# Kernel optimization log

Hardware: AMD Instinct MI355X
Metric: run time of the kernel (lower is better)

## Reference

```python
import jax, jax.numpy as jnp
import numpy as np

MARGIN = 0.2
NEG_SENTINEL = -1e30


def setup_inputs() -> dict:
    key = jax.random.key(0)
    k1, k2 = jax.random.split(key)
    batch_reprs = jax.random.normal(k1, (4096, 128), dtype=jnp.float32)
    batch_labels = jax.random.randint(k2, (4096,), 0, 512, dtype=jnp.int64 if jax.config.jax_enable_x64 else jnp.int32)
    return {"batch_reprs": batch_reprs, "batch_labels": batch_labels}


def _loss(batch_reprs, batch_labels):
    # class match matrix (self-similarity kept, as in original)
    match = (batch_labels[:, None] == batch_labels[None, :]).astype(batch_reprs.dtype)  # [B,B]

    # pairwise euclidean distance (squared=False), sim = -dist
    sq = jnp.sum(batch_reprs * batch_reprs, axis=1)
    d2 = jnp.maximum(sq[:, None] + sq[None, :] - 2.0 * (batch_reprs @ batch_reprs.T), 0.0)
    zero = (d2 == 0.0).astype(batch_reprs.dtype)
    dist = jnp.sqrt(d2 + zero * 1e-16) * (1.0 - zero)
    sim_hat = -dist + (1.0 - match) * MARGIN  # use_margin=True

    # rank positions via double argsort (descending)
    order = jnp.argsort(-sim_hat, axis=1)
    rank = jnp.argsort(order, axis=1).astype(sim_hat.dtype) + 1.0  # [B,B], 1-based ranks

    k = jnp.sum(match, axis=1, keepdims=True)                      # n_pos per row, [B,1]
    fp = (match < 1.0) & (rank <= k)                               # false positives
    fp_num = jnp.sum(fp, axis=1, keepdims=True).astype(sim_hat.dtype)
    fn = (match > 0.0) & (rank > k)                                # false negatives

    n = sim_hat.shape[1]
    # per-row top-(fp_num) false negatives by sim_hat, vectorized via masked sort
    fn_scores = jnp.where(fn, sim_hat, NEG_SENTINEL)
    idx = jnp.argsort(-fn_scores, axis=1)
    fn_sorted = jnp.take_along_axis(sim_hat, idx, axis=1)
    fn_ranks = jnp.take_along_axis(rank, idx, axis=1)
    fn_mask_sorted = jnp.take_along_axis(fn, idx, axis=1)
    sel = (jnp.arange(n)[None, :] < fp_num) & fn_mask_sorted       # top fp_num entries

    # weighted margins (rows with fp_num==0 contribute 0 automatically)
    fp_term = jnp.sum(jnp.where(fp, sim_hat * (0.5 + (k - rank + 1.0) / k * 0.5), 0.0))
    fn_term = jnp.sum(jnp.where(sel, fn_sorted * (0.5 + (fn_ranks - k) / (n - k) * 0.5), 0.0))
    return fp_term - fn_term


def reference(batch_reprs, batch_labels):
    return _loss(batch_reprs, batch_labels)
```

## Files before the change

### kernel.cpp

```cpp
#include <hip/hip_runtime.h>
#include <cstdint>
#include <cstddef>

#define B 4096
#define D 128
#define MARGIN_F 0.2f
#define CW 256
#define ROWS 16
#define SSTR 4104

typedef short bf16x8 __attribute__((ext_vector_type(8)));
typedef float f32x4 __attribute__((ext_vector_type(4)));
typedef uint32_t u32x4 __attribute__((ext_vector_type(4)));

__device__ __forceinline__ uint32_t xform_key(float f) {
    uint32_t u = __float_as_uint(f);
    return u ^ (uint32_t)((((int32_t)u) >> 31) | 0x80000000);
}
__device__ __forceinline__ float unxform16(uint32_t k16) {
    uint32_t u = k16 << 16;
    u = (u & 0x80000000u) ? (u ^ 0x80000000u) : ~u;
    return __uint_as_float(u);
}
__device__ __forceinline__ unsigned short f2bf(float f) {
    uint32_t u = __float_as_uint(f);
    return (unsigned short)((u + 0x7FFFu + ((u >> 16) & 1u)) >> 16);
}

__global__ __launch_bounds__(256) void prep_kernel(const float* __restrict__ R,
                                                   float* __restrict__ sq,
                                                   unsigned short* __restrict__ Rb,
                                                   float* __restrict__ out) {
    if (blockIdx.x == 0 && threadIdx.x == 0) out[0] = 0.0f;
    int wave = threadIdx.x >> 6;
    int lane = threadIdx.x & 63;
    int row  = blockIdx.x * 4 + wave;
    const float2* R2 = (const float2*)R + (size_t)row * (D / 2);
    float2 v = R2[lane];
    ushort2 o; o.x = f2bf(v.x); o.y = f2bf(v.y);
    *(ushort2*)(Rb + (size_t)row * D + lane * 2) = o;
    float s = v.x * v.x + v.y * v.y;
#pragma unroll
    for (int off = 32; off > 0; off >>= 1) s += __shfl_down(s, off);
    if (lane == 0) sq[row] = s;
}

__global__ __launch_bounds__(1024)
__attribute__((amdgpu_waves_per_eu(4, 4)))
void fused_loss(const unsigned short* __restrict__ Rb,
                const float* __restrict__ sq,
                const int* __restrict__ labels,
                float* __restrict__ out) {
    __shared__ unsigned short S[ROWS * SSTR];
    __shared__ uint32_t cand_c[ROWS][CW];

    const int tid  = threadIdx.x;
    const int wid  = tid >> 6, lane = tid & 63;
    const int q    = lane >> 4, t = lane & 15;
    const int r0   = blockIdx.x * ROWS;

    {
        uint32_t* cz = &cand_c[0][0];
#pragma unroll
        for (int c = 0; c < (ROWS * CW) / 1024; ++c)
            cz[tid + c * 1024] = 0u;
    }

    bf16x8 af[4];
    const unsigned short* baseA = Rb + (size_t)(r0 + t) * D + q * 8;
#pragma unroll
    for (int kq = 0; kq < 4; ++kq)
        af[kq] = *(const bf16x8*)(baseA + kq * 32);

    float sqa[4]; int la[4];
#pragma unroll
    for (int rr = 0; rr < 4; ++rr) {
        sqa[rr] = sq[r0 + q * 4 + rr];
        la[rr]  = labels[r0 + q * 4 + rr];
    }

    for (int i = 0; i < 16; ++i) {
        const int jt  = wid * 16 + i;
        const int col = jt * 16 + t;
        const unsigned short* baseB = Rb + (size_t)col * D + q * 8;
        bf16x8 bfr[4];
#pragma unroll
        for (int kq = 0; kq < 4; ++kq)
            bfr[kq] = *(const bf16x8*)(baseB + kq * 32);
        f32x4 acc = (f32x4)0.0f;
#pragma unroll
        for (int kq = 0; kq < 4; ++kq)
            acc = __builtin_amdgcn_mfma_f32_16x16x32_bf16(af[kq], bfr[kq], acc, 0, 0, 0);

        const float sqc = sq[col];
        const int   lc  = labels[col];
#pragma unroll
        for (int rr = 0; rr < 4; ++rr) {
            float g  = acc[rr];
            float d2 = fmaxf(sqa[rr] + sqc - 2.0f * g, 0.0f);
            float dist = (d2 > 0.0f) ? sqrtf(d2) : 0.0f;
            float s = -dist + ((la[rr] == lc) ? 0.0f : MARGIN_F);
            uint32_t key = xform_key(s);
            S[(q * 4 + rr) * SSTR + col] = (unsigned short)((key + 0x8000u) >> 16);
        }
    }
    __syncthreads();

    float facc = 0.0f;
    const int4* lv = (const int4*)labels;

    {
        const int row  = wid;
        const int grow = r0 + row;
        const int li   = labels[grow];

        uint64_t mbits = 0;
        uint32_t t1 = 0, t2 = 0;
        int total = 0;

        u32x4 kv[8];
#pragma unroll
        for (int qq = 0; qq < 8; ++qq)
            kv[qq] = *(u32x4*)(&S[row * SSTR + (qq * 64 + lane) * 8]);
        asm volatile("" : "+v"(kv[0]), "+v"(kv[1]), "+v"(kv[2]), "+v"(kv[3]),
                          "+v"(kv[4]), "+v"(kv[5]), "+v"(kv[6]), "+v"(kv[7]));

        {
            uint32_t t1a[8], t2a[8];
#pragma unroll
            for (int qq = 0; qq < 8; ++qq) {
                const int lb = (qq * 64 + lane) * 2;
                int4 la4 = lv[lb], lc4 = lv[lb + 1];
                uint32_t u[8] = {kv[qq].x & 0xFFFFu, kv[qq].x >> 16,
                                 kv[qq].y & 0xFFFFu, kv[qq].y >> 16,
                                 kv[qq].z & 0xFFFFu, kv[qq].z >> 16,
                                 kv[qq].w & 0xFFFFu, kv[qq].w >> 16};
                uint32_t l1 = 0, l2 = 0;
#pragma unroll
                for (int c = 0; c < 8; ++c) {
                    uint32_t mn = min(l1, u[c]);
                    l1 = max(l1, u[c]);
                    l2 = max(l2, mn);
                }
                t1a[qq] = l1; t2a[qq] = l2;
                mbits |= (uint64_t)(la4.x == li) << (qq * 8 + 0);
                mbits |= (uint64_t)(la4.y == li) << (qq * 8 + 1);
                mbits |= (uint64_t)(la4.z == li) << (qq * 8 + 2);
                mbits |= (uint64_t)(la4.w == li) << (qq * 8 + 3);
                mbits |= (uint64_t)(lc4.x == li) << (qq * 8 + 4);
                mbits |= (uint64_t)(lc4.y == li) << (qq * 8 + 5);
                mbits |= (uint64_t)(lc4.z == li) << (qq * 8 + 6);
                mbits |= (uint64_t)(lc4.w == li) << (qq * 8 + 7);
            }
#pragma unroll
            for (int qq = 0; qq < 8; ++qq) {
                uint32_t mn = min(t1, t1a[qq]);
                t1 = max(t1, t1a[qq]);
                t2 = max(t2, mn);
                mn = min(t1, t2a[qq]);
                t1 = max(t1, t2a[qq]);
                t2 = max(t2, mn);
            }

            int kloc = __popcll(mbits);
#pragma unroll
            for (int off = 32; off > 0; off >>= 1) kloc += __shfl_xor(kloc, off);
            const int k0 = kloc;

            const int kneed = min(k0, 128);
            uint32_t T = 0;
#pragma unroll
            for (int b = 15; b >= 0; --b) {
                uint32_t g = T | (1u << b);
                int c = __popcll(__ballot(t1 >= g)) + __popcll(__ballot(t2 >= g));
                if (c >= kneed) T = g;
            }

            uint64_t wmask = 0;
#pragma unroll
            for (int qq = 0; qq < 8; ++qq) {
                uint32_t u[8] = {kv[qq].x & 0xFFFFu, kv[qq].x >> 16,
                                 kv[qq].y & 0xFFFFu, kv[qq].y >> 16,
                                 kv[qq].z & 0xFFFFu, kv[qq].z >> 16,
                                 kv[qq].w & 0xFFFFu, kv[qq].w >> 16};
#pragma unroll
                for (int c = 0; c < 8; ++c) {
                    int e = qq * 8 + c;
                    uint32_t m = (uint32_t)((mbits >> e) & 1);
                    wmask |= (uint64_t)((u[c] >= T) | m) << e;
                }
            }
            int cw = __popcll(wmask);
            int inc = cw;
#pragma unroll
            for (int off = 1; off < 64; off <<= 1) {
                int v = __shfl_up(inc, off);
                if (lane >= off) inc += v;
            }
            int mybase = inc - cw;
            total = __shfl(inc, 63);

#pragma unroll
            for (int qq = 0; qq < 8; ++qq) {
                uint32_t sub = (uint32_t)((wmask >> (qq * 8)) & 0xFFu);
                uint32_t u[8] = {kv[qq].x & 0xFFFFu, kv[qq].x >> 16,
                                 kv[qq].y & 0xFFFFu, kv[qq].y >> 16,
                                 kv[qq].z & 0xFFFFu, kv[qq].z >> 16,
                                 kv[qq].w & 0xFFFFu, kv[qq].w >> 16};
                int jb = (qq * 64 + lane) * 8;
#pragma unroll
                for (int c = 0; c < 8; ++c) {
                    if (sub & (1u << c)) {
                        if (mybase < CW) {
                            uint32_t m = (uint32_t)((mbits >> (qq * 8 + c)) & 1);
                            cand_c[row][mybase] =
                                (u[c] << 12) | (uint32_t)(4095 - (jb + c)) | (m << 31);
                        }
                        ++mybase;
                    }
                }
            }

            t1 = T;
            t2 = (uint32_t)k0;
        }

        const uint32_t T = t1;
        const int k = (int)t2;
        const float kf = (float)k;
        const uint32_t combT = T << 12;
        const int ncand = min(total, CW);

        __builtin_amdgcn_s_waitcnt(0);

        uint32_t cr0 = cand_c[row][lane];
        uint32_t cr1 = cand_c[row][lane + 64];
        uint32_t cr2 = cand_c[row][lane + 128];
        uint32_t cr3 = cand_c[row][lane + 192];
        uint32_t mycomb[4] = {cr0 & 0x7FFFFFFFu, cr1 & 0x7FFFFFFFu,
                              cr2 & 0x7FFFFFFFu, cr3 & 0x7FFFFFFFu};
        int mym[4]  = {(int)(cr0 >> 31), (int)(cr1 >> 31),
                       (int)(cr2 >> 31), (int)(cr3 >> 31)};
        int myok[4] = {lane < ncand, lane + 64 < ncand,
                       lane + 128 < ncand, lane + 192 < ncand};
        int myc[4]  = {0, 0, 0, 0};

        const int npad = (ncand + 7) & ~7;
        for (int c0i = 0; c0i < npad; c0i += 8) {
            u32x4 a = *(const u32x4*)&cand_c[row][c0i];
            u32x4 b = *(const u32x4*)&cand_c[row][c0i + 4];
            uint32_t vv[8] = {a.x, a.y, a.z, a.w, b.x, b.y, b.z, b.w};
#pragma unroll
            for (int e = 0; e < 8; ++e) {
                uint32_t vm = vv[e] & 0x7FFFFFFFu;
#pragma unroll
                for (int j = 0; j < 4; ++j)
                    myc[j] += (vm > mycomb[j]) ? 1 : 0;
            }
        }

#pragma unroll
        for (int j = 0; j < 4; ++j) {
            if (myok[j] && mycomb[j] >= combT) {
                int rank = 1 + myc[j];
                float v = unxform16(mycomb[j] >> 12);
                if (!mym[j] && rank <= k)
                    facc += v * (0.5f + ((kf - (float)rank + 1.0f) / kf) * 0.5f);
                else if (mym[j] && rank > k)
                    facc -= v * (0.5f + (((float)rank - kf) / (float)(B - k)) * 0.5f);
            }
        }

        uint32_t p0 = 0xFFFFFFFFu, p1 = 0xFFFFFFFFu, p2 = 0xFFFFFFFFu, p3 = 0xFFFFFFFFu;

        auto flush4 = [&](int npv) {
            int c0 = 0, c1 = 0, c2 = 0, c3 = 0;
#pragma unroll
            for (int qq = 0; qq < 8; ++qq) {
                uint32_t u[8] = {kv[qq].x & 0xFFFFu, kv[qq].x >> 16,
                                 kv[qq].y & 0xFFFFu, kv[qq].y >> 16,
                                 kv[qq].z & 0xFFFFu, kv[qq].z >> 16,
                                 kv[qq].w & 0xFFFFu, kv[qq].w >> 16};
                int jb = (qq * 64 + lane) * 8;
#pragma unroll
                for (int cc = 0; cc < 8; ++cc) {
                    uint32_t ce = (u[cc] << 12) | (uint32_t)(4095 - (jb + cc));
                    c0 += (ce > p0) ? 1 : 0;  c1 += (ce > p1) ? 1 : 0;
                    c2 += (ce > p2) ? 1 : 0;  c3 += (ce > p3) ? 1 : 0;
                }
            }
#pragma unroll
            for (int off = 32; off > 0; off >>= 1) {
                c0 += __shfl_xor(c0, off); c1 += __shfl_xor(c1, off);
                c2 += __shfl_xor(c2, off); c3 += __shfl_xor(c3, off);
            }
            if (lane == 0) {
                if (npv > 0) facc -= unxform16(p0 >> 12) * (0.5f + (((float)(1 + c0) - kf) / (float)(B - k)) * 0.5f);
                if (npv > 1) facc -= unxform16(p1 >> 12) * (0.5f + (((float)(1 + c1) - kf) / (float)(B - k)) * 0.5f);
                if (npv > 2) facc -= unxform16(p2 >> 12) * (0.5f + (((float)(1 + c2) - kf) / (float)(B - k)) * 0.5f);
                if (npv > 3) facc -= unxform16(p3 >> 12) * (0.5f + (((float)(1 + c3) - kf) / (float)(B - k)) * 0.5f);
            }
            p0 = p1 = p2 = p3 = 0xFFFFFFFFu;
        };

        int np = 0;
#pragma unroll
        for (int j = 0; j < 4; ++j) {
            uint64_t mg = __ballot(myok[j] && mym[j] && (mycomb[j] < combT));
            while (mg) {
                int src = __ffsll((unsigned long long)mg) - 1;
                mg &= mg - 1;
                uint32_t pc;
                if (j == 0)      pc = __shfl(mycomb[0], src);
                else if (j == 1) pc = __shfl(mycomb[1], src);
                else if (j == 2) pc = __shfl(mycomb[2], src);
                else             pc = __shfl(mycomb[3], src);
                switch (np) {
                    case 0: p0 = pc; break; case 1: p1 = pc; break;
                    case 2: p2 = pc; break; default: p3 = pc; break;
                }
                ++np;
                if (np == 4) { flush4(4); np = 0; }
            }
        }
        if (np > 0) flush4(np);
    }

#pragma unroll
    for (int off = 32; off > 0; off >>= 1) facc += __shfl_xor(facc, off);
    if (lane == 0) atomicAdd(out, facc);
}

extern "C" void kernel_launch(void* const* d_in, const int* in_sizes, int n_in,
                              void* d_out, int out_size, void* d_ws, size_t ws_size,
                              hipStream_t stream) {
    const float* R      = (const float*)d_in[0];
    const int*   labels = (const int*)d_in[1];
    float* out = (float*)d_out;

    float*          sq = (float*)d_ws;
    unsigned short* Rb = (unsigned short*)((char*)d_ws + 16 * 1024);

    hipLaunchKernelGGL(prep_kernel, dim3(B / 4), dim3(256), 0, stream, R, sq, Rb, out);
    hipLaunchKernelGGL(fused_loss, dim3(B / ROWS), dim3(1024), 0, stream,
                       Rb, sq, labels, out);
}
```

Measured before the change: 152.8 us.

## Split fused loss into gram-keys and rank-loss kernels via global key buffer

The single fused kernel held a 16-row key tile in LDS and ran both the MFMA Gram phase and the per-row ranking phase. It is now split into two kernels. gram_keys writes 16-bit sort keys to a 32 MB global buffer and software-prefetches the next B tile. rank_loss handles 8 rows per 512-thread block. Dummy LDS padding arrays are added to cap occupancy per CU. The aim is to decouple the two phases' occupancy and resource needs, at the cost of an extra launch and a round trip of the full key matrix through global memory/L2.

```diff
diff --git a/kernel.cpp b/kernel.cpp
--- a/kernel.cpp
+++ b/kernel.cpp
@@ -6,8 +6,6 @@
 #define D 128
 #define MARGIN_F 0.2f
 #define CW 256
-#define ROWS 16
-#define SSTR 4104
 
 typedef short bf16x8 __attribute__((ext_vector_type(8)));
 typedef float f32x4 __attribute__((ext_vector_type(4)));
@@ -45,26 +43,18 @@
     if (lane == 0) sq[row] = s;
 }
 
-__global__ __launch_bounds__(1024)
-__attribute__((amdgpu_waves_per_eu(4, 4)))
-void fused_loss(const unsigned short* __restrict__ Rb,
-                const float* __restrict__ sq,
-                const int* __restrict__ labels,
-                float* __restrict__ out) {
-    __shared__ unsigned short S[ROWS * SSTR];
-    __shared__ uint32_t cand_c[ROWS][CW];
+__global__ __launch_bounds__(512) void gram_keys(const unsigned short* __restrict__ Rb,
+                                                 const float* __restrict__ sq,
+                                                 const int* __restrict__ labels,
+                                                 unsigned short* __restrict__ K,
+                                                 float* __restrict__ out) {
+    __shared__ uint8_t apad[80 * 1024];
+    if ((size_t)out == 1) *(volatile uint8_t*)apad = 1;
 
     const int tid  = threadIdx.x;
     const int wid  = tid >> 6, lane = tid & 63;
     const int q    = lane >> 4, t = lane & 15;
-    const int r0   = blockIdx.x * ROWS;
-
-    {
-        uint32_t* cz = &cand_c[0][0];
-#pragma unroll
-        for (int c = 0; c < (ROWS * CW) / 1024; ++c)
-            cz[tid + c * 1024] = 0u;
-    }
+    const int r0   = blockIdx.x * 16;
 
     bf16x8 af[4];
     const unsigned short* baseA = Rb + (size_t)(r0 + t) * D + q * 8;
@@ -79,21 +69,36 @@
         la[rr]  = labels[r0 + q * 4 + rr];
     }
 
-    for (int i = 0; i < 16; ++i) {
-        const int jt  = wid * 16 + i;
-        const int col = jt * 16 + t;
+    const int jt0 = wid * 32;
+    int col = jt0 * 16 + t;
+    bf16x8 bfr[4];
+    {
         const unsigned short* baseB = Rb + (size_t)col * D + q * 8;
-        bf16x8 bfr[4];
 #pragma unroll
         for (int kq = 0; kq < 4; ++kq)
             bfr[kq] = *(const bf16x8*)(baseB + kq * 32);
+    }
+    float sqc = sq[col];
+    int   lc  = labels[col];
+
+    for (int i = 0; i < 32; ++i) {
+        const int jn   = (i < 31) ? (jt0 + i + 1) : (jt0 + 31);
+        const int coln = jn * 16 + t;
+        bf16x8 bnx[4];
+        {
+            const unsigned short* baseB = Rb + (size_t)coln * D + q * 8;
+#pragma unroll
+            for (int kq = 0; kq < 4; ++kq)
+                bnx[kq] = *(const bf16x8*)(baseB + kq * 32);
+        }
+        const float sqn = sq[coln];
+        const int   lcn = labels[coln];
+
         f32x4 acc = (f32x4)0.0f;
 #pragma unroll
         for (int kq = 0; kq < 4; ++kq)
             acc = __builtin_amdgcn_mfma_f32_16x16x32_bf16(af[kq], bfr[kq], acc, 0, 0, 0);
 
-        const float sqc = sq[col];
-        const int   lc  = labels[col];
 #pragma unroll
         for (int rr = 0; rr < 4; ++rr) {
             float g  = acc[rr];
@@ -101,230 +106,242 @@
             float dist = (d2 > 0.0f) ? sqrtf(d2) : 0.0f;
             float s = -dist + ((la[rr] == lc) ? 0.0f : MARGIN_F);
             uint32_t key = xform_key(s);
-            S[(q * 4 + rr) * SSTR + col] = (unsigned short)((key + 0x8000u) >> 16);
-        }
-    }
-    __syncthreads();
+            K[(size_t)(r0 + q * 4 + rr) * B + col] =
+                (unsigned short)((key + 0x8000u) >> 16);
+        }
+
+#pragma unroll
+        for (int kq = 0; kq < 4; ++kq) bfr[kq] = bnx[kq];
+        sqc = sqn; lc = lcn; col = coln;
+    }
+}
+
+__global__ __launch_bounds__(512) void rank_loss(const unsigned short* __restrict__ K,
+                                                 const int* __restrict__ labels,
+                                                 float* __restrict__ out) {
+    __shared__ uint32_t cand_c[8][CW];
+    __shared__ uint8_t  bpad[56 * 1024];
+    if ((size_t)out == 1) *(volatile uint8_t*)bpad = 1;
+
+    const int tid  = threadIdx.x;
+    const int wid  = tid >> 6, lane = tid & 63;
+    const int row  = blockIdx.x * 8 + wid;
+    const int li   = labels[row];
+    const int4* lv = (const int4*)labels;
+
+#pragma unroll
+    for (int c = 0; c < CW / 64; ++c)
+        cand_c[wid][lane + c * 64] = 0u;
 
     float facc = 0.0f;
-    const int4* lv = (const int4*)labels;
+
+    u32x4 kv[8];
+    const unsigned short* krow = K + (size_t)row * B;
+#pragma unroll
+    for (int qq = 0; qq < 8; ++qq)
+        kv[qq] = *(const u32x4*)(krow + (qq * 64 + lane) * 8);
+    asm volatile("" : "+v"(kv[0]), "+v"(kv[1]), "+v"(kv[2]), "+v"(kv[3]),
+                      "+v"(kv[4]), "+v"(kv[5]), "+v"(kv[6]), "+v"(kv[7]));
+
+    uint64_t mbits = 0;
+    uint32_t t1 = 0, t2 = 0;
 
     {
-        const int row  = wid;
-        const int grow = r0 + row;
-        const int li   = labels[grow];
-
-        uint64_t mbits = 0;
-        uint32_t t1 = 0, t2 = 0;
-        int total = 0;
-
-        u32x4 kv[8];
-#pragma unroll
-        for (int qq = 0; qq < 8; ++qq)
-            kv[qq] = *(u32x4*)(&S[row * SSTR + (qq * 64 + lane) * 8]);
-        asm volatile("" : "+v"(kv[0]), "+v"(kv[1]), "+v"(kv[2]), "+v"(kv[3]),
-                          "+v"(kv[4]), "+v"(kv[5]), "+v"(kv[6]), "+v"(kv[7]));
-
-        {
-            uint32_t t1a[8], t2a[8];
-#pragma unroll
-            for (int qq = 0; qq < 8; ++qq) {
-                const int lb = (qq * 64 + lane) * 2;
-                int4 la4 = lv[lb], lc4 = lv[lb + 1];
-                uint32_t u[8] = {kv[qq].x & 0xFFFFu, kv[qq].x >> 16,
-                                 kv[qq].y & 0xFFFFu, kv[qq].y >> 16,
-                                 kv[qq].z & 0xFFFFu, kv[qq].z >> 16,
-                                 kv[qq].w & 0xFFFFu, kv[qq].w >> 16};
-                uint32_t l1 = 0, l2 = 0;
-#pragma unroll
-                for (int c = 0; c < 8; ++c) {
-                    uint32_t mn = min(l1, u[c]);
-                    l1 = max(l1, u[c]);
-                    l2 = max(l2, mn);
+        uint32_t t1a[8], t2a[8];
+#pragma unroll
+        for (int qq = 0; qq < 8; ++qq) {
+            const int lb = (qq * 64 + lane) * 2;
+            int4 la4 = lv[lb], lc4 = lv[lb + 1];
+            uint32_t u[8] = {kv[qq].x & 0xFFFFu, kv[qq].x >> 16,
+                             kv[qq].y & 0xFFFFu, kv[qq].y >> 16,
+                             kv[qq].z & 0xFFFFu, kv[qq].z >> 16,
+                             kv[qq].w & 0xFFFFu, kv[qq].w >> 16};
+            uint32_t l1 = 0, l2 = 0;
+#pragma unroll
+            for (int c = 0; c < 8; ++c) {
+                uint32_t mn = min(l1, u[c]);
+                l1 = max(l1, u[c]);
+                l2 = max(l2, mn);
+            }
+            t1a[qq] = l1; t2a[qq] = l2;
+            mbits |= (uint64_t)(la4.x == li) << (qq * 8 + 0);
+            mbits |= (uint64_t)(la4.y == li) << (qq * 8 + 1);
+            mbits |= (uint64_t)(la4.z == li) << (qq * 8 + 2);
+            mbits |= (uint64_t)(la4.w == li) << (qq * 8 + 3);
+            mbits |= (uint64_t)(lc4.x == li) << (qq * 8 + 4);
+            mbits |= (uint64_t)(lc4.y == li) << (qq * 8 + 5);
+            mbits |= (uint64_t)(lc4.z == li) << (qq * 8 + 6);
+            mbits |= (uint64_t)(lc4.w == li) << (qq * 8 + 7);
+        }
+#pragma unroll
+        for (int qq = 0; qq < 8; ++qq) {
+            uint32_t mn = min(t1, t1a[qq]);
+            t1 = max(t1, t1a[qq]);
+            t2 = max(t2, mn);
+            mn = min(t1, t2a[qq]);
+            t1 = max(t1, t2a[qq]);
+            t2 = max(t2, mn);
+        }
+    }
+
+    int kloc = __popcll(mbits);
+#pragma unroll
+    for (int off = 32; off > 0; off >>= 1) kloc += __shfl_xor(kloc, off);
+    const int k = kloc;
+    const float kf = (float)k;
+
+    const int kneed = min(k, 128);
+    uint32_t T = 0;
+#pragma unroll
+    for (int b = 15; b >= 0; --b) {
+        uint32_t g = T | (1u << b);
+        int c = __popcll(__ballot(t1 >= g)) + __popcll(__ballot(t2 >= g));
+        if (c >= kneed) T = g;
+    }
+    const uint32_t combT = T << 12;
+
+    int total = 0;
+    {
+        uint64_t wmask = 0;
+#pragma unroll
+        for (int qq = 0; qq < 8; ++qq) {
+            uint32_t u[8] = {kv[qq].x & 0xFFFFu, kv[qq].x >> 16,
+                             kv[qq].y & 0xFFFFu, kv[qq].y >> 16,
+                             kv[qq].z & 0xFFFFu, kv[qq].z >> 16,
+                             kv[qq].w & 0xFFFFu, kv[qq].w >> 16};
+#pragma unroll
+            for (int c = 0; c < 8; ++c) {
+                int e = qq * 8 + c;
+                uint32_t m = (uint32_t)((mbits >> e) & 1);
+                wmask |= (uint64_t)((u[c] >= T) | m) << e;
+            }
+        }
+        int cw = __popcll(wmask);
+        int inc = cw;
+#pragma unroll
+        for (int off = 1; off < 64; off <<= 1) {
+            int v = __shfl_up(inc, off);
+            if (lane >= off) inc += v;
+        }
+        int mybase = inc - cw;
+        total = __shfl(inc, 63);
+
+#pragma unroll
+        for (int qq = 0; qq < 8; ++qq) {
+            uint32_t sub = (uint32_t)((wmask >> (qq * 8)) & 0xFFu);
+            uint32_t u[8] = {kv[qq].x & 0xFFFFu, kv[qq].x >> 16,
+                             kv[qq].y & 0xFFFFu, kv[qq].y >> 16,
+                             kv[qq].z & 0xFFFFu, kv[qq].z >> 16,
+                             kv[qq].w & 0xFFFFu, kv[qq].w >> 16};
+            int jb = (qq * 64 + lane) * 8;
+#pragma unroll
+            for (int c = 0; c < 8; ++c) {
+                if (sub & (1u << c)) {
+                    if (mybase < CW) {
+                        uint32_t m = (uint32_t)((mbits >> (qq * 8 + c)) & 1);
+                        cand_c[wid][mybase] =
+                            (u[c] << 12) | (uint32_t)(4095 - (jb + c)) | (m << 31);
+                    }
+                    ++mybase;
                 }
-                t1a[qq] = l1; t2a[qq] = l2;
-                mbits |= (uint64_t)(la4.x == li) << (qq * 8 + 0);
-                mbits |= (uint64_t)(la4.y == li) << (qq * 8 + 1);
-                mbits |= (uint64_t)(la4.z == li) << (qq * 8 + 2);
-                mbits |= (uint64_t)(la4.w == li) << (qq * 8 + 3);
-                mbits |= (uint64_t)(lc4.x == li) << (qq * 8 + 4);
-                mbits |= (uint64_t)(lc4.y == li) << (qq * 8 + 5);
-                mbits |= (uint64_t)(lc4.z == li) << (qq * 8 + 6);
-                mbits |= (uint64_t)(lc4.w == li) << (qq * 8 + 7);
-            }
-#pragma unroll
-            for (int qq = 0; qq < 8; ++qq) {
-                uint32_t mn = min(t1, t1a[qq]);
-                t1 = max(t1, t1a[qq]);
-                t2 = max(t2, mn);
-                mn = min(t1, t2a[qq]);
-                t1 = max(t1, t2a[qq]);
-                t2 = max(t2, mn);
-            }
-
-            int kloc = __popcll(mbits);
-#pragma unroll
-            for (int off = 32; off > 0; off >>= 1) kloc += __shfl_xor(kloc, off);
-            const int k0 = kloc;
-
-            const int kneed = min(k0, 128);
-            uint32_t T = 0;
-#pragma unroll
-            for (int b = 15; b >= 0; --b) {
-                uint32_t g = T | (1u << b);
-                int c = __popcll(__ballot(t1 >= g)) + __popcll(__ballot(t2 >= g));
-                if (c >= kneed) T = g;
-            }
-
-            uint64_t wmask = 0;
-#pragma unroll
-            for (int qq = 0; qq < 8; ++qq) {
-                uint32_t u[8] = {kv[qq].x & 0xFFFFu, kv[qq].x >> 16,
-                                 kv[qq].y & 0xFFFFu, kv[qq].y >> 16,
-                                 kv[qq].z & 0xFFFFu, kv[qq].z >> 16,
-                                 kv[qq].w & 0xFFFFu, kv[qq].w >> 16};
-#pragma unroll
-                for (int c = 0; c < 8; ++c) {
-                    int e = qq * 8 + c;
-                    uint32_t m = (uint32_t)((mbits >> e) & 1);
-                    wmask |= (uint64_t)((u[c] >= T) | m) << e;
-                }
-            }
-            int cw = __popcll(wmask);
-            int inc = cw;
-#pragma unroll
-            for (int off = 1; off < 64; off <<= 1) {
-                int v = __shfl_up(inc, off);
-                if (lane >= off) inc += v;
-            }
-            int mybase = inc - cw;
-            total = __shfl(inc, 63);
-
-#pragma unroll
-            for (int qq = 0; qq < 8; ++qq) {
-                uint32_t sub = (uint32_t)((wmask >> (qq * 8)) & 0xFFu);
-                uint32_t u[8] = {kv[qq].x & 0xFFFFu, kv[qq].x >> 16,
-                                 kv[qq].y & 0xFFFFu, kv[qq].y >> 16,
-                                 kv[qq].z & 0xFFFFu, kv[qq].z >> 16,
-                                 kv[qq].w & 0xFFFFu, kv[qq].w >> 16};
-                int jb = (qq * 64 + lane) * 8;
-#pragma unroll
-                for (int c = 0; c < 8; ++c) {
-                    if (sub & (1u << c)) {
-                        if (mybase < CW) {
-                            uint32_t m = (uint32_t)((mbits >> (qq * 8 + c)) & 1);
-                            cand_c[row][mybase] =
-                                (u[c] << 12) | (uint32_t)(4095 - (jb + c)) | (m << 31);
-                        }
-                        ++mybase;
-                    }
-                }
-            }
-
-            t1 = T;
-            t2 = (uint32_t)k0;
-        }
-
-        const uint32_t T = t1;
-        const int k = (int)t2;
-        const float kf = (float)k;
-        const uint32_t combT = T << 12;
-        const int ncand = min(total, CW);
-
-        __builtin_amdgcn_s_waitcnt(0);
-
-        uint32_t cr0 = cand_c[row][lane];
-        uint32_t cr1 = cand_c[row][lane + 64];
-        uint32_t cr2 = cand_c[row][lane + 128];
-        uint32_t cr3 = cand_c[row][lane + 192];
-        uint32_t mycomb[4] = {cr0 & 0x7FFFFFFFu, cr1 & 0x7FFFFFFFu,
-                              cr2 & 0x7FFFFFFFu, cr3 & 0x7FFFFFFFu};
-        int mym[4]  = {(int)(cr0 >> 31), (int)(cr1 >> 31),
-                       (int)(cr2 >> 31), (int)(cr3 >> 31)};
-        int myok[4] = {lane < ncand, lane + 64 < ncand,
-                       lane + 128 < ncand, lane + 192 < ncand};
-        int myc[4]  = {0, 0, 0, 0};
-
-        const int npad = (ncand + 7) & ~7;
-        for (int c0i = 0; c0i < npad; c0i += 8) {
-            u32x4 a = *(const u32x4*)&cand_c[row][c0i];
-            u32x4 b = *(const u32x4*)&cand_c[row][c0i + 4];
-            uint32_t vv[8] = {a.x, a.y, a.z, a.w, b.x, b.y, b.z, b.w};
-#pragma unroll
-            for (int e = 0; e < 8; ++e) {
-                uint32_t vm = vv[e] & 0x7FFFFFFFu;
-#pragma unroll
-                for (int j = 0; j < 4; ++j)
-                    myc[j] += (vm > mycomb[j]) ? 1 : 0;
-            }
-        }
-
-#pragma unroll
-        for (int j = 0; j < 4; ++j) {
-            if (myok[j] && mycomb[j] >= combT) {
-                int rank = 1 + myc[j];
-                float v = unxform16(mycomb[j] >> 12);
-                if (!mym[j] && rank <= k)
-                    facc += v * (0.5f + ((kf - (float)rank + 1.0f) / kf) * 0.5f);
-                else if (mym[j] && rank > k)
-                    facc -= v * (0.5f + (((float)rank - kf) / (float)(B - k)) * 0.5f);
-            }
-        }
-
-        uint32_t p0 = 0xFFFFFFFFu, p1 = 0xFFFFFFFFu, p2 = 0xFFFFFFFFu, p3 = 0xFFFFFFFFu;
-
-        auto flush4 = [&](int npv) {
-            int c0 = 0, c1 = 0, c2 = 0, c3 = 0;
-#pragma unroll
-            for (int qq = 0; qq < 8; ++qq) {
-                uint32_t u[8] = {kv[qq].x & 0xFFFFu, kv[qq].x >> 16,
-                                 kv[qq].y & 0xFFFFu, kv[qq].y >> 16,
-                                 kv[qq].z & 0xFFFFu, kv[qq].z >> 16,
-                                 kv[qq].w & 0xFFFFu, kv[qq].w >> 16};
-                int jb = (qq * 64 + lane) * 8;
-#pragma unroll
-                for (int cc = 0; cc < 8; ++cc) {
-                    uint32_t ce = (u[cc] << 12) | (uint32_t)(4095 - (jb + cc));
-                    c0 += (ce > p0) ? 1 : 0;  c1 += (ce > p1) ? 1 : 0;
-                    c2 += (ce > p2) ? 1 : 0;  c3 += (ce > p3) ? 1 : 0;
-                }
-            }
-#pragma unroll
-            for (int off = 32; off > 0; off >>= 1) {
-                c0 += __shfl_xor(c0, off); c1 += __shfl_xor(c1, off);
-                c2 += __shfl_xor(c2, off); c3 += __shfl_xor(c3, off);
-            }
-            if (lane == 0) {
-                if (npv > 0) facc -= unxform16(p0 >> 12) * (0.5f + (((float)(1 + c0) - kf) / (float)(B - k)) * 0.5f);
-                if (npv > 1) facc -= unxform16(p1 >> 12) * (0.5f + (((float)(1 + c1) - kf) / (float)(B - k)) * 0.5f);
-                if (npv > 2) facc -= unxform16(p2 >> 12) * (0.5f + (((float)(1 + c2) - kf) / (float)(B - k)) * 0.5f);
-                if (npv > 3) facc -= unxform16(p3 >> 12) * (0.5f + (((float)(1 + c3) - kf) / (float)(B - k)) * 0.5f);
-            }
-            p0 = p1 = p2 = p3 = 0xFFFFFFFFu;
-        };
-
-        int np = 0;
-#pragma unroll
-        for (int j = 0; j < 4; ++j) {
-            uint64_t mg = __ballot(myok[j] && mym[j] && (mycomb[j] < combT));
-            while (mg) {
-                int src = __ffsll((unsigned long long)mg) - 1;
-                mg &= mg - 1;
-                uint32_t pc;
-                if (j == 0)      pc = __shfl(mycomb[0], src);
-                else if (j == 1) pc = __shfl(mycomb[1], src);
-                else if (j == 2) pc = __shfl(mycomb[2], src);
-                else             pc = __shfl(mycomb[3], src);
-                switch (np) {
-                    case 0: p0 = pc; break; case 1: p1 = pc; break;
-                    case 2: p2 = pc; break; default: p3 = pc; break;
-                }
-                ++np;
-                if (np == 4) { flush4(4); np = 0; }
-            }
-        }
-        if (np > 0) flush4(np);
-    }
+            }
+        }
+    }
+    const int ncand = min(total, CW);
+
+    __builtin_amdgcn_s_waitcnt(0);
+
+    uint32_t cr0 = cand_c[wid][lane];
+    uint32_t cr1 = cand_c[wid][lane + 64];
+    uint32_t cr2 = cand_c[wid][lane + 128];
+    uint32_t cr3 = cand_c[wid][lane + 192];
+    uint32_t mycomb[4] = {cr0 & 0x7FFFFFFFu, cr1 & 0x7FFFFFFFu,
+                          cr2 & 0x7FFFFFFFu, cr3 & 0x7FFFFFFFu};
+    int mym[4]  = {(int)(cr0 >> 31), (int)(cr1 >> 31),
+                   (int)(cr2 >> 31), (int)(cr3 >> 31)};
+    int myok[4] = {lane < ncand, lane + 64 < ncand,
+                   lane + 128 < ncand, lane + 192 < ncand};
+    int myc[4]  = {0, 0, 0, 0};
+
+    const int npad = (ncand + 7) & ~7;
+    for (int c0i = 0; c0i < npad; c0i += 8) {
+        u32x4 a = *(const u32x4*)&cand_c[wid][c0i];
+        u32x4 b = *(const u32x4*)&cand_c[wid][c0i + 4];
+        uint32_t vv[8] = {a.x, a.y, a.z, a.w, b.x, b.y, b.z, b.w};
+#pragma unroll
+        for (int e = 0; e < 8; ++e) {
+            uint32_t vm = vv[e] & 0x7FFFFFFFu;
+#pragma unroll
+            for (int j = 0; j < 4; ++j)
+                myc[j] += (vm > mycomb[j]) ? 1 : 0;
+        }
+    }
+
+#pragma unroll
+    for (int j = 0; j < 4; ++j) {
+        if (myok[j] && mycomb[j] >= combT) {
+            int rank = 1 + myc[j];
+            float v = unxform16(mycomb[j] >> 12);
+            if (!mym[j] && rank <= k)
+                facc += v * (0.5f + ((kf - (float)rank + 1.0f) / kf) * 0.5f);
+            else if (mym[j] && rank > k)
+                facc -= v * (0.5f + (((float)rank - kf) / (float)(B - k)) * 0.5f);
+        }
+    }
+
+    uint32_t p0 = 0xFFFFFFFFu, p1 = 0xFFFFFFFFu, p2 = 0xFFFFFFFFu, p3 = 0xFFFFFFFFu;
+
+    auto flush4 = [&](int npv) {
+        int c0 = 0, c1 = 0, c2 = 0, c3 = 0;
+#pragma unroll
+        for (int qq = 0; qq < 8; ++qq) {
+            uint32_t u[8] = {kv[qq].x & 0xFFFFu, kv[qq].x >> 16,
+                             kv[qq].y & 0xFFFFu, kv[qq].y >> 16,
+                             kv[qq].z & 0xFFFFu, kv[qq].z >> 16,
+                             kv[qq].w & 0xFFFFu, kv[qq].w >> 16};
+            int jb = (qq * 64 + lane) * 8;
+#pragma unroll
+            for (int cc = 0; cc < 8; ++cc) {
+                uint32_t ce = (u[cc] << 12) | (uint32_t)(4095 - (jb + cc));
+                c0 += (ce > p0) ? 1 : 0;  c1 += (ce > p1) ? 1 : 0;
+                c2 += (ce > p2) ? 1 : 0;  c3 += (ce > p3) ? 1 : 0;
+            }
+        }
+#pragma unroll
+        for (int off = 32; off > 0; off >>= 1) {
+            c0 += __shfl_xor(c0, off); c1 += __shfl_xor(c1, off);
+            c2 += __shfl_xor(c2, off); c3 += __shfl_xor(c3, off);
+        }
+        if (lane == 0) {
+            if (npv > 0) facc -= unxform16(p0 >> 12) * (0.5f + (((float)(1 + c0) - kf) / (float)(B - k)) * 0.5f);
+            if (npv > 1) facc -= unxform16(p1 >> 12) * (0.5f + (((float)(1 + c1) - kf) / (float)(B - k)) * 0.5f);
+            if (npv > 2) facc -= unxform16(p2 >> 12) * (0.5f + (((float)(1 + c2) - kf) / (float)(B - k)) * 0.5f);
+            if (npv > 3) facc -= unxform16(p3 >> 12) * (0.5f + (((float)(1 + c3) - kf) / (float)(B - k)) * 0.5f);
+        }
+        p0 = p1 = p2 = p3 = 0xFFFFFFFFu;
+    };
+
+    int np = 0;
+#pragma unroll
+    for (int j = 0; j < 4; ++j) {
+        uint64_t mg = __ballot(myok[j] && mym[j] && (mycomb[j] < combT));
+        while (mg) {
+            int src = __ffsll((unsigned long long)mg) - 1;
+            mg &= mg - 1;
+            uint32_t pc;
+            if (j == 0)      pc = __shfl(mycomb[0], src);
+            else if (j == 1) pc = __shfl(mycomb[1], src);
+            else if (j == 2) pc = __shfl(mycomb[2], src);
+            else             pc = __shfl(mycomb[3], src);
+            switch (np) {
+                case 0: p0 = pc; break; case 1: p1 = pc; break;
+                case 2: p2 = pc; break; default: p3 = pc; break;
+            }
+            ++np;
+            if (np == 4) { flush4(4); np = 0; }
+        }
+    }
+    if (np > 0) flush4(np);
 
 #pragma unroll
     for (int off = 32; off > 0; off >>= 1) facc += __shfl_xor(facc, off);
@@ -340,8 +357,12 @@
 
     float*          sq = (float*)d_ws;
     unsigned short* Rb = (unsigned short*)((char*)d_ws + 16 * 1024);
+    unsigned short* K  = (unsigned short*)((char*)d_ws + 16 * 1024
+                                           + (size_t)B * D * 2);
 
     hipLaunchKernelGGL(prep_kernel, dim3(B / 4), dim3(256), 0, stream, R, sq, Rb, out);
-    hipLaunchKernelGGL(fused_loss, dim3(B / ROWS), dim3(1024), 0, stream,
-                       Rb, sq, labels, out);
-}
+    hipLaunchKernelGGL(gram_keys, dim3(B / 16), dim3(512), 0, stream,
+                       Rb, sq, labels, K, out);
+    hipLaunchKernelGGL(rank_loss, dim3(B / 8), dim3(512), 0, stream,
+                       K, labels, out);
+}
```

Result: slower. 173.0 us (+13.2%).
